# Kernel optimization log

Measured on AMD Instinct MI355X. Metric: run time of the kernel, lower is better.

The kernel has to match this reference:

```python
import jax, jax.numpy as jnp
import numpy as np

N = 200000          # nodes
E = 12_800_000      # edges (avg degree 64)
C = 4               # conv_out_channels == node_features
H = 32              # lstm_out_channels


def setup_inputs() -> dict:
    key = jax.random.key(0)
    ks = jax.random.split(key, 16)
    inv_c = 1.0 / np.sqrt(C)
    inv_h = 1.0 / np.sqrt(H)
    return {
        "x": jax.random.normal(ks[0], (N, C), jnp.float32),
        "edge_index": jax.random.randint(ks[1], (2, E), 0, N, dtype=jnp.int64),
        "edge_weight": jax.random.uniform(ks[2], (E,), jnp.float32),
        "h_0": 0.1 * jax.random.normal(ks[3], (1, N, H), jnp.float32),
        "c_0": 0.1 * jax.random.normal(ks[4], (1, N, H), jnp.float32),
        # GatedGraphConv (num_layers=1): weight[0] of shape [C, C]
        "conv_weight": inv_c * jax.random.normal(ks[5], (C, C), jnp.float32),
        # GRUCell(C, C) params (PyTorch layout: [3C, C], gate order r,z,n)
        "gru_w_ih": inv_c * jax.random.normal(ks[6], (3 * C, C), jnp.float32),
        "gru_w_hh": inv_c * jax.random.normal(ks[7], (3 * C, C), jnp.float32),
        "gru_b_ih": inv_c * jax.random.normal(ks[8], (3 * C,), jnp.float32),
        "gru_b_hh": inv_c * jax.random.normal(ks[9], (3 * C,), jnp.float32),
        # LSTM(C, H, 1 layer) params (PyTorch layout: [4H, *], gate order i,f,g,o)
        "lstm_w_ih": inv_h * jax.random.normal(ks[10], (4 * H, C), jnp.float32),
        "lstm_w_hh": inv_h * jax.random.normal(ks[11], (4 * H, H), jnp.float32),
        "lstm_b_ih": inv_h * jax.random.normal(ks[12], (4 * H,), jnp.float32),
        "lstm_b_hh": inv_h * jax.random.normal(ks[13], (4 * H,), jnp.float32),
        # Linear(32, 1)
        "lin_w": inv_h * jax.random.normal(ks[14], (1, H), jnp.float32),
        "lin_b": inv_h * jax.random.normal(ks[15], (1,), jnp.float32),
    }


def reference(x, edge_index, edge_weight, h_0, c_0,
              conv_weight, gru_w_ih, gru_w_hh, gru_b_ih, gru_b_hh,
              lstm_w_ih, lstm_w_hh, lstm_b_ih, lstm_b_hh, lin_w, lin_b):
    n = x.shape[0]
    src, dst = edge_index[0], edge_index[1]  # source j -> target i

    # ---- GatedGraphConv, 1 layer (in_dim == out_channels, no padding) ----
    m = x @ conv_weight                                   # [N, C]
    msg = m[src] * edge_weight[:, None]                   # [E, C] gather
    summed = jax.ops.segment_sum(msg, dst, num_segments=n)
    cnt = jax.ops.segment_sum(jnp.ones((msg.shape[0],), msg.dtype), dst,
                              num_segments=n)
    agg = summed / jnp.maximum(cnt, 1.0)[:, None]         # mean aggr (empty -> 0)

    # GRUCell(agg, x): r,z,n gate order
    gi = agg @ gru_w_ih.T + gru_b_ih
    gh = x @ gru_w_hh.T + gru_b_hh
    i_r, i_z, i_n = jnp.split(gi, 3, axis=1)
    h_r, h_z, h_n = jnp.split(gh, 3, axis=1)
    r = jax.nn.sigmoid(i_r + h_r)
    z = jax.nn.sigmoid(i_z + h_z)
    nn_ = jnp.tanh(i_n + r * h_n)
    h_conv = (1.0 - z) * nn_ + z * x                      # [N, C]

    # ---- LSTM: seq_len=1, batch=N, 1 layer; gate order i,f,g,o ----
    h_prev, c_prev = h_0[0], c_0[0]                       # [N, H]
    gates = h_conv @ lstm_w_ih.T + lstm_b_ih + h_prev @ lstm_w_hh.T + lstm_b_hh
    ig, fg, gg, og = jnp.split(gates, 4, axis=1)
    ig, fg, og = jax.nn.sigmoid(ig), jax.nn.sigmoid(fg), jax.nn.sigmoid(og)
    gg = jnp.tanh(gg)
    c_new = fg * c_prev + ig * gg
    h_new = og * jnp.tanh(c_new)                          # [N, H]

    # ---- relu + linear head ----
    out = jax.nn.relu(h_new) @ lin_w.T + lin_b            # [N, 1]
    return out, h_new[None], c_new[None]
```

## Files before the change

### kernel.cpp

```cpp
#include <hip/hip_runtime.h>
#include <math.h>

#define B_SHIFT 9
#define BMASK   511
#define CHUNK   16384
#define NTHR    256
#define AGG_THR 512

static __device__ __forceinline__ float sigf(float x) {
  return 1.0f / (1.0f + __expf(-x));
}
static __device__ __forceinline__ float tanhfast(float x) {
  return 2.0f / (1.0f + __expf(-2.0f * x)) - 1.0f;
}

__global__ void conv_m_kernel(const float* __restrict__ x,
                              const float* __restrict__ w,
                              float* __restrict__ m, int n) {
  int i = blockIdx.x * blockDim.x + threadIdx.x;
  if (i >= n) return;
  float4 xv = reinterpret_cast<const float4*>(x)[i];
  float4 mv;
  mv.x = xv.x * w[0] + xv.y * w[4] + xv.z * w[8]  + xv.w * w[12];
  mv.y = xv.x * w[1] + xv.y * w[5] + xv.z * w[9]  + xv.w * w[13];
  mv.z = xv.x * w[2] + xv.y * w[6] + xv.z * w[10] + xv.w * w[14];
  mv.w = xv.x * w[3] + xv.y * w[7] + xv.z * w[11] + xv.w * w[15];
  reinterpret_cast<float4*>(m)[i] = mv;
}


__global__ __launch_bounds__(NTHR) void hist_kernel(const int* __restrict__ dst,
                                                    int E, int B,
                                                    int* __restrict__ gCnt) {
  __shared__ int h[1024];
  for (int b = threadIdx.x; b < B; b += NTHR) h[b] = 0;
  __syncthreads();
  const int4* d4 = reinterpret_cast<const int4*>(dst);
  int i4base = (int)(((long long)blockIdx.x * CHUNK) >> 2);
  int lim4 = E >> 2;
#pragma unroll
  for (int j = 0; j < 16; ++j) {
    int i4 = i4base + j * NTHR + threadIdx.x;
    if (i4 < lim4) {
      int4 d = d4[i4];
      atomicAdd(&h[d.x >> B_SHIFT], 1);
      atomicAdd(&h[d.y >> B_SHIFT], 1);
      atomicAdd(&h[d.z >> B_SHIFT], 1);
      atomicAdd(&h[d.w >> B_SHIFT], 1);
    }
  }
  if (blockIdx.x == 0 && threadIdx.x == 0) {
    for (int e = E & ~3; e < E; ++e) atomicAdd(&h[dst[e] >> B_SHIFT], 1);
  }
  __syncthreads();
  for (int b = threadIdx.x; b < B; b += NTHR) {
    int c = h[b];
    if (c) atomicAdd(&gCnt[b], c);
  }
}

__global__ void scan_kernel(const int* __restrict__ gCnt, int B,
                            int* __restrict__ start, int* __restrict__ cursor) {
  __shared__ int s[1024];
  int t = threadIdx.x;
  int v = (t < B) ? gCnt[t] : 0;
  s[t] = v;
  __syncthreads();
  for (int off = 1; off < 1024; off <<= 1) {
    int u = (t >= off) ? s[t - off] : 0;
    __syncthreads();
    s[t] += u;
    __syncthreads();
  }
  if (t < B) {
    int excl = (t == 0) ? 0 : s[t - 1];
    start[t] = excl;
    cursor[t] = excl;
  }
  if (t == 0) start[B] = s[1023];
}

__global__ __launch_bounds__(NTHR) void bin_kernel(const int* __restrict__ ei,
                                                   const float* __restrict__ ew,
                                                   int E, int B,
                                                   int* __restrict__ cursor,
                                                   int2* __restrict__ binned) {
  __shared__ int h[1024];
  for (int b = threadIdx.x; b < B; b += NTHR) h[b] = 0;
  __syncthreads();
  const int* dst = ei + E;
  const int4* d4 = reinterpret_cast<const int4*>(dst);
  const int4* s4 = reinterpret_cast<const int4*>(ei);
  const float4* w4 = reinterpret_cast<const float4*>(ew);
  int i4base = (int)(((long long)blockIdx.x * CHUNK) >> 2);
  int lim4 = E >> 2;
#pragma unroll
  for (int j = 0; j < 16; ++j) {
    int i4 = i4base + j * NTHR + threadIdx.x;
    if (i4 < lim4) {
      int4 d = d4[i4];
      atomicAdd(&h[d.x >> B_SHIFT], 1);
      atomicAdd(&h[d.y >> B_SHIFT], 1);
      atomicAdd(&h[d.z >> B_SHIFT], 1);
      atomicAdd(&h[d.w >> B_SHIFT], 1);
    }
  }
  __syncthreads();
  for (int b = threadIdx.x; b < B; b += NTHR) {
    int c = h[b];
    if (c) h[b] = atomicAdd(&cursor[b], c);
  }
  __syncthreads();
#pragma unroll
  for (int j = 0; j < 16; ++j) {
    int i4 = i4base + j * NTHR + threadIdx.x;
    if (i4 < lim4) {
      int4 d = d4[i4];
      int4 s = s4[i4];
      float4 w = w4[i4];
      int p;
      p = atomicAdd(&h[d.x >> B_SHIFT], 1);
      binned[p] = make_int2((s.x << B_SHIFT) | (d.x & BMASK), __float_as_int(w.x));
      p = atomicAdd(&h[d.y >> B_SHIFT], 1);
      binned[p] = make_int2((s.y << B_SHIFT) | (d.y & BMASK), __float_as_int(w.y));
      p = atomicAdd(&h[d.z >> B_SHIFT], 1);
      binned[p] = make_int2((s.z << B_SHIFT) | (d.z & BMASK), __float_as_int(w.z));
      p = atomicAdd(&h[d.w >> B_SHIFT], 1);
      binned[p] = make_int2((s.w << B_SHIFT) | (d.w & BMASK), __float_as_int(w.w));
    }
  }
  if (blockIdx.x == 0 && threadIdx.x == 0) {
    for (int e = E & ~3; e < E; ++e) {
      int d = dst[e];
      int p = atomicAdd(&cursor[d >> B_SHIFT], 1);
      binned[p] = make_int2((ei[e] << B_SHIFT) | (d & BMASK), __float_as_int(ew[e]));
    }
  }
}

__global__ __launch_bounds__(AGG_THR) void agg_node_kernel(
    const float* __restrict__ x, const float* __restrict__ m,
    const int2* __restrict__ binned, const int* __restrict__ start,
    const float* __restrict__ h0, const float* __restrict__ c0,
    const float* __restrict__ gwi, const float* __restrict__ gwh,
    const float* __restrict__ gbi, const float* __restrict__ gbh,
    const float* __restrict__ lwi, const float* __restrict__ lwh,
    const float* __restrict__ lbi, const float* __restrict__ lbh,
    const float* __restrict__ linw, const float* __restrict__ linb,
    float* __restrict__ out, float* __restrict__ hout, float* __restrict__ cout,
    int n) {
  __shared__ float acc[512 * 5];
  int tid = threadIdx.x;
  for (int idx = tid; idx < 512 * 5; idx += AGG_THR) acc[idx] = 0.0f;
  __syncthreads();

  int s = start[blockIdx.x], e = start[blockIdx.x + 1];
  const float4* m4 = reinterpret_cast<const float4*>(m);
  int i = s + tid;
  for (; i + AGG_THR < e; i += 2 * AGG_THR) {
    int2 r0 = binned[i];
    int2 r1 = binned[i + AGG_THR];
    float4 mv0 = m4[r0.x >> B_SHIFT];
    float4 mv1 = m4[r1.x >> B_SHIFT];
    float w0 = __int_as_float(r0.y);
    float w1 = __int_as_float(r1.y);
    int dl0 = (r0.x & BMASK) * 5;
    int dl1 = (r1.x & BMASK) * 5;
    atomicAdd(&acc[dl0 + 0], mv0.x * w0);
    atomicAdd(&acc[dl0 + 1], mv0.y * w0);
    atomicAdd(&acc[dl0 + 2], mv0.z * w0);
    atomicAdd(&acc[dl0 + 3], mv0.w * w0);
    atomicAdd(&acc[dl0 + 4], 1.0f);
    atomicAdd(&acc[dl1 + 0], mv1.x * w1);
    atomicAdd(&acc[dl1 + 1], mv1.y * w1);
    atomicAdd(&acc[dl1 + 2], mv1.z * w1);
    atomicAdd(&acc[dl1 + 3], mv1.w * w1);
    atomicAdd(&acc[dl1 + 4], 1.0f);
  }
  if (i < e) {
    int2 r = binned[i];
    int src = r.x >> B_SHIFT;
    int dl = (r.x & BMASK) * 5;
    float w = __int_as_float(r.y);
    float4 mv = m4[src];
    atomicAdd(&acc[dl + 0], mv.x * w);
    atomicAdd(&acc[dl + 1], mv.y * w);
    atomicAdd(&acc[dl + 2], mv.z * w);
    atomicAdd(&acc[dl + 3], mv.w * w);
    atomicAdd(&acc[dl + 4], 1.0f);
  }
  __syncthreads();

  int node = (blockIdx.x << B_SHIFT) + tid;
  if (node >= n) return;

  float inv = 1.0f / fmaxf(acc[tid * 5 + 4], 1.0f);
  float agg[4] = {acc[tid * 5 + 0] * inv, acc[tid * 5 + 1] * inv,
                  acc[tid * 5 + 2] * inv, acc[tid * 5 + 3] * inv};
  float4 xv = reinterpret_cast<const float4*>(x)[node];
  float xa[4] = {xv.x, xv.y, xv.z, xv.w};

  float hc[4];
#pragma unroll
  for (int c = 0; c < 4; ++c) {
    float gi_r = gbi[c],     gh_r = gbh[c];
    float gi_z = gbi[4 + c], gh_z = gbh[4 + c];
    float gi_n = gbi[8 + c], gh_n = gbh[8 + c];
#pragma unroll
    for (int k = 0; k < 4; ++k) {
      gi_r += agg[k] * gwi[c * 4 + k];       gh_r += xa[k] * gwh[c * 4 + k];
      gi_z += agg[k] * gwi[(4 + c) * 4 + k]; gh_z += xa[k] * gwh[(4 + c) * 4 + k];
      gi_n += agg[k] * gwi[(8 + c) * 4 + k]; gh_n += xa[k] * gwh[(8 + c) * 4 + k];
    }
    float r = sigf(gi_r + gh_r);
    float z = sigf(gi_z + gh_z);
    float nn = tanhfast(gi_n + r * gh_n);
    hc[c] = (1.0f - z) * nn + z * xa[c];
  }

  const float4* h04 = reinterpret_cast<const float4*>(h0) + (size_t)node * 8;
  const float4* c04 = reinterpret_cast<const float4*>(c0) + (size_t)node * 8;
  float hp[32];
#pragma unroll
  for (int q = 0; q < 8; ++q) {
    float4 hv = h04[q];
    hp[q * 4 + 0] = hv.x; hp[q * 4 + 1] = hv.y;
    hp[q * 4 + 2] = hv.z; hp[q * 4 + 3] = hv.w;
  }
  const float4* wih4 = reinterpret_cast<const float4*>(lwi);
  const float4* whh4 = reinterpret_cast<const float4*>(lwh);
  float oacc = linb[0];
  float4* hout4 = reinterpret_cast<float4*>(hout) + (size_t)node * 8;
  float4* cout4 = reinterpret_cast<float4*>(cout) + (size_t)node * 8;

#pragma unroll
  for (int jc = 0; jc < 8; ++jc) {
    float4 cpv = c04[jc];
    float cpa[4] = {cpv.x, cpv.y, cpv.z, cpv.w};
    float hn[4], cn[4];
#pragma unroll
    for (int jj = 0; jj < 4; ++jj) {
      int j = jc * 4 + jj;
      float gI = lbi[j]      + lbh[j];
      float gF = lbi[32 + j] + lbh[32 + j];
      float gG = lbi[64 + j] + lbh[64 + j];
      float gO = lbi[96 + j] + lbh[96 + j];
      float4 wi = wih4[j], wf = wih4[32 + j], wg = wih4[64 + j], wo = wih4[96 + j];
      gI += hc[0] * wi.x + hc[1] * wi.y + hc[2] * wi.z + hc[3] * wi.w;
      gF += hc[0] * wf.x + hc[1] * wf.y + hc[2] * wf.z + hc[3] * wf.w;
      gG += hc[0] * wg.x + hc[1] * wg.y + hc[2] * wg.z + hc[3] * wg.w;
      gO += hc[0] * wo.x + hc[1] * wo.y + hc[2] * wo.z + hc[3] * wo.w;
#pragma unroll
      for (int q = 0; q < 8; ++q) {
        float4 a = whh4[j * 8 + q];
        float4 b = whh4[(32 + j) * 8 + q];
        float4 g = whh4[(64 + j) * 8 + q];
        float4 o = whh4[(96 + j) * 8 + q];
        float p0 = hp[q * 4 + 0], p1 = hp[q * 4 + 1];
        float p2 = hp[q * 4 + 2], p3 = hp[q * 4 + 3];
        gI += p0 * a.x + p1 * a.y + p2 * a.z + p3 * a.w;
        gF += p0 * b.x + p1 * b.y + p2 * b.z + p3 * b.w;
        gG += p0 * g.x + p1 * g.y + p2 * g.z + p3 * g.w;
        gO += p0 * o.x + p1 * o.y + p2 * o.z + p3 * o.w;
      }
      float ig = sigf(gI), fg = sigf(gF), og = sigf(gO), gg = tanhfast(gG);
      float cnew = fg * cpa[jj] + ig * gg;
      float hnew = og * tanhfast(cnew);
      cn[jj] = cnew; hn[jj] = hnew;
      oacc += fmaxf(hnew, 0.0f) * linw[j];
    }
    hout4[jc] = make_float4(hn[0], hn[1], hn[2], hn[3]);
    cout4[jc] = make_float4(cn[0], cn[1], cn[2], cn[3]);
  }
  out[node] = oacc;
}


__global__ void edge_kernel(const int* __restrict__ ei,
                            const float* __restrict__ ew,
                            const float* __restrict__ m,
                            float* __restrict__ summed,
                            float* __restrict__ cnt, int E) {
  int t = blockIdx.x * blockDim.x + threadIdx.x;
  int e0 = t * 4;
  const float4* m4 = reinterpret_cast<const float4*>(m);
  for (int e = e0; e < E && e < e0 + 4; ++e) {
    int s = ei[e], d = ei[E + e];
    float w = ew[e];
    float4 mv = m4[s];
    float* p = summed + 4ll * d;
    unsafeAtomicAdd(p + 0, mv.x * w);
    unsafeAtomicAdd(p + 1, mv.y * w);
    unsafeAtomicAdd(p + 2, mv.z * w);
    unsafeAtomicAdd(p + 3, mv.w * w);
    unsafeAtomicAdd(cnt + d, 1.0f);
  }
}

__global__ __launch_bounds__(NTHR) void node_kernel(
    const float* __restrict__ x, const float* __restrict__ summed,
    const float* __restrict__ cnt,
    const float* __restrict__ h0, const float* __restrict__ c0,
    const float* __restrict__ gwi, const float* __restrict__ gwh,
    const float* __restrict__ gbi, const float* __restrict__ gbh,
    const float* __restrict__ lwi, const float* __restrict__ lwh,
    const float* __restrict__ lbi, const float* __restrict__ lbh,
    const float* __restrict__ linw, const float* __restrict__ linb,
    float* __restrict__ out, float* __restrict__ hout, float* __restrict__ cout,
    int n) {
  int i = blockIdx.x * blockDim.x + threadIdx.x;
  if (i >= n) return;
  float4 sv = reinterpret_cast<const float4*>(summed)[i];
  float inv = 1.0f / fmaxf(cnt[i], 1.0f);
  float agg[4] = {sv.x * inv, sv.y * inv, sv.z * inv, sv.w * inv};
  float4 xv = reinterpret_cast<const float4*>(x)[i];
  float xa[4] = {xv.x, xv.y, xv.z, xv.w};
  float hc[4];
#pragma unroll
  for (int c = 0; c < 4; ++c) {
    float gi_r = gbi[c],     gh_r = gbh[c];
    float gi_z = gbi[4 + c], gh_z = gbh[4 + c];
    float gi_n = gbi[8 + c], gh_n = gbh[8 + c];
#pragma unroll
    for (int k = 0; k < 4; ++k) {
      gi_r += agg[k] * gwi[c * 4 + k];       gh_r += xa[k] * gwh[c * 4 + k];
      gi_z += agg[k] * gwi[(4 + c) * 4 + k]; gh_z += xa[k] * gwh[(4 + c) * 4 + k];
      gi_n += agg[k] * gwi[(8 + c) * 4 + k]; gh_n += xa[k] * gwh[(8 + c) * 4 + k];
    }
    float r = sigf(gi_r + gh_r);
    float z = sigf(gi_z + gh_z);
    float nn = tanhfast(gi_n + r * gh_n);
    hc[c] = (1.0f - z) * nn + z * xa[c];
  }
  const float4* h04 = reinterpret_cast<const float4*>(h0) + (size_t)i * 8;
  const float4* c04 = reinterpret_cast<const float4*>(c0) + (size_t)i * 8;
  float hp[32];
#pragma unroll
  for (int q = 0; q < 8; ++q) {
    float4 hv = h04[q];
    hp[q * 4 + 0] = hv.x; hp[q * 4 + 1] = hv.y;
    hp[q * 4 + 2] = hv.z; hp[q * 4 + 3] = hv.w;
  }
  const float4* wih4 = reinterpret_cast<const float4*>(lwi);
  const float4* whh4 = reinterpret_cast<const float4*>(lwh);
  float oacc = linb[0];
  float4* hout4 = reinterpret_cast<float4*>(hout) + (size_t)i * 8;
  float4* cout4 = reinterpret_cast<float4*>(cout) + (size_t)i * 8;
#pragma unroll
  for (int jc = 0; jc < 8; ++jc) {
    float4 cpv = c04[jc];
    float cpa[4] = {cpv.x, cpv.y, cpv.z, cpv.w};
    float hn[4], cn[4];
#pragma unroll
    for (int jj = 0; jj < 4; ++jj) {
      int j = jc * 4 + jj;
      float gI = lbi[j]      + lbh[j];
      float gF = lbi[32 + j] + lbh[32 + j];
      float gG = lbi[64 + j] + lbh[64 + j];
      float gO = lbi[96 + j] + lbh[96 + j];
      float4 wi = wih4[j], wf = wih4[32 + j], wg = wih4[64 + j], wo = wih4[96 + j];
      gI += hc[0] * wi.x + hc[1] * wi.y + hc[2] * wi.z + hc[3] * wi.w;
      gF += hc[0] * wf.x + hc[1] * wf.y + hc[2] * wf.z + hc[3] * wf.w;
      gG += hc[0] * wg.x + hc[1] * wg.y + hc[2] * wg.z + hc[3] * wg.w;
      gO += hc[0] * wo.x + hc[1] * wo.y + hc[2] * wo.z + hc[3] * wo.w;
#pragma unroll
      for (int q = 0; q < 8; ++q) {
        float4 a = whh4[j * 8 + q];
        float4 b = whh4[(32 + j) * 8 + q];
        float4 g = whh4[(64 + j) * 8 + q];
        float4 o = whh4[(96 + j) * 8 + q];
        float p0 = hp[q * 4 + 0], p1 = hp[q * 4 + 1];
        float p2 = hp[q * 4 + 2], p3 = hp[q * 4 + 3];
        gI += p0 * a.x + p1 * a.y + p2 * a.z + p3 * a.w;
        gF += p0 * b.x + p1 * b.y + p2 * b.z + p3 * b.w;
        gG += p0 * g.x + p1 * g.y + p2 * g.z + p3 * g.w;
        gO += p0 * o.x + p1 * o.y + p2 * o.z + p3 * o.w;
      }
      float ig = sigf(gI), fg = sigf(gF), og = sigf(gO), gg = tanhfast(gG);
      float cnew = fg * cpa[jj] + ig * gg;
      float hnew = og * tanhfast(cnew);
      cn[jj] = cnew; hn[jj] = hnew;
      oacc += fmaxf(hnew, 0.0f) * linw[j];
    }
    hout4[jc] = make_float4(hn[0], hn[1], hn[2], hn[3]);
    cout4[jc] = make_float4(cn[0], cn[1], cn[2], cn[3]);
  }
  out[i] = oacc;
}

extern "C" void kernel_launch(void* const* d_in, const int* in_sizes, int n_in,
                              void* d_out, int out_size, void* d_ws, size_t ws_size,
                              hipStream_t stream) {
  const float* x     = (const float*)d_in[0];
  const int*   ei    = (const int*)d_in[1];
  const float* ew    = (const float*)d_in[2];
  const float* h0    = (const float*)d_in[3];
  const float* c0    = (const float*)d_in[4];
  const float* convw = (const float*)d_in[5];
  const float* gwi   = (const float*)d_in[6];
  const float* gwh   = (const float*)d_in[7];
  const float* gbi   = (const float*)d_in[8];
  const float* gbh   = (const float*)d_in[9];
  const float* lwi   = (const float*)d_in[10];
  const float* lwh   = (const float*)d_in[11];
  const float* lbi   = (const float*)d_in[12];
  const float* lbh   = (const float*)d_in[13];
  const float* linw  = (const float*)d_in[14];
  const float* linb  = (const float*)d_in[15];

  int n = in_sizes[0] / 4;
  int E = in_sizes[1] / 2;

  float* out  = (float*)d_out;
  float* hout = out + n;
  float* cout = hout + (size_t)n * 32;

  int B = (n + BMASK) >> B_SHIFT;
  size_t need = (size_t)E * 8 + (size_t)n * 16 + ((size_t)3 * B + 2) * 4 + 64;

  if (B <= 1024 && ws_size >= need) {
    int2*  binned = (int2*)d_ws;
    float* m      = (float*)(binned + E);
    int*   gCnt   = (int*)(m + (size_t)n * 4);
    int*   start  = gCnt + B;
    int*   cursor = start + B + 1;

    hipMemsetAsync(gCnt, 0, (size_t)B * sizeof(int), stream);
    conv_m_kernel<<<(n + NTHR - 1) / NTHR, NTHR, 0, stream>>>(x, convw, m, n);

    int nbBlocks = (E + CHUNK - 1) / CHUNK;
    hist_kernel<<<nbBlocks, NTHR, 0, stream>>>(ei + E, E, B, gCnt);
    scan_kernel<<<1, 1024, 0, stream>>>(gCnt, B, start, cursor);
    bin_kernel<<<nbBlocks, NTHR, 0, stream>>>(ei, ew, E, B, cursor, binned);

    agg_node_kernel<<<B, AGG_THR, 0, stream>>>(
        x, m, binned, start, h0, c0,
        gwi, gwh, gbi, gbh, lwi, lwh, lbi, lbh, linw, linb,
        out, hout, cout, n);
  } else {
    float* m      = (float*)d_ws;
    float* summed = m + (size_t)n * 4;
    float* cntp   = summed + (size_t)n * 4;
    hipMemsetAsync(summed, 0, (size_t)n * 5 * sizeof(float), stream);
    conv_m_kernel<<<(n + NTHR - 1) / NTHR, NTHR, 0, stream>>>(x, convw, m, n);
    int et = (E + 3) / 4;
    edge_kernel<<<(et + NTHR - 1) / NTHR, NTHR, 0, stream>>>(ei, ew, m, summed, cntp, E);
    node_kernel<<<(n + NTHR - 1) / NTHR, NTHR, 0, stream>>>(
        x, summed, cntp, h0, c0,
        gwi, gwh, gbi, gbh, lwi, lwh, lbi, lbh, linw, linb,
        out, hout, cout, n);
  }
}
```

Before: 1.058 ms.

## Split fused edge-aggregation/LSTM kernel and halve bin size for more blocks

Splits the fused aggregation-plus-node-update kernel into an LDS-atomic edge aggregation kernel writing mean aggregates to workspace and a separate per-node GRU/LSTM kernel. Bin size drops from 512 to 256 nodes, doubling the number of aggregation blocks, with a 4-way unrolled edge loop and workgroup-scoped relaxed LDS atomics. This targets low block count and occupancy limits from the register-heavy LSTM tail sharing a kernel with the atomics loop. It costs an extra global write/read of the aggregate array, one more launch, and more bins in the histogram/scan.

```diff
diff --git a/kernel.cpp b/kernel.cpp
--- a/kernel.cpp
+++ b/kernel.cpp
@@ -1,11 +1,13 @@
 #include <hip/hip_runtime.h>
 #include <math.h>
 
-#define B_SHIFT 9
-#define BMASK   511
+#define B_SHIFT 8
+#define BMASK   255
 #define CHUNK   16384
 #define NTHR    256
-#define AGG_THR 512
+
+#define LDSADD(p, v) __hip_atomic_fetch_add((p), (v), __ATOMIC_RELAXED, \
+                                            __HIP_MEMORY_SCOPE_WORKGROUP)
 
 static __device__ __forceinline__ float sigf(float x) {
   return 1.0f / (1.0f + __expf(-x));
@@ -138,9 +140,65 @@
   }
 }
 
-__global__ __launch_bounds__(AGG_THR) void agg_node_kernel(
-    const float* __restrict__ x, const float* __restrict__ m,
-    const int2* __restrict__ binned, const int* __restrict__ start,
+__global__ __launch_bounds__(NTHR) void edge_agg_kernel(
+    const float* __restrict__ m, const int2* __restrict__ binned,
+    const int* __restrict__ start, float* __restrict__ aggOut, int n) {
+  __shared__ float acc[NTHR * 5];
+  int tid = threadIdx.x;
+#pragma unroll
+  for (int k = 0; k < 5; ++k) acc[k * NTHR + tid] = 0.0f;
+  __syncthreads();
+
+  int s = start[blockIdx.x], e = start[blockIdx.x + 1];
+  const float4* m4 = reinterpret_cast<const float4*>(m);
+  int i = s + tid;
+  for (; i + 3 * NTHR < e; i += 4 * NTHR) {
+    int2 r0 = binned[i];
+    int2 r1 = binned[i + NTHR];
+    int2 r2 = binned[i + 2 * NTHR];
+    int2 r3 = binned[i + 3 * NTHR];
+    float4 v0 = m4[r0.x >> B_SHIFT];
+    float4 v1 = m4[r1.x >> B_SHIFT];
+    float4 v2 = m4[r2.x >> B_SHIFT];
+    float4 v3 = m4[r3.x >> B_SHIFT];
+    float w0 = __int_as_float(r0.y), w1 = __int_as_float(r1.y);
+    float w2 = __int_as_float(r2.y), w3 = __int_as_float(r3.y);
+    int a0 = (r0.x & BMASK) * 5, a1 = (r1.x & BMASK) * 5;
+    int a2 = (r2.x & BMASK) * 5, a3 = (r3.x & BMASK) * 5;
+    LDSADD(&acc[a0 + 0], v0.x * w0); LDSADD(&acc[a0 + 1], v0.y * w0);
+    LDSADD(&acc[a0 + 2], v0.z * w0); LDSADD(&acc[a0 + 3], v0.w * w0);
+    LDSADD(&acc[a0 + 4], 1.0f);
+    LDSADD(&acc[a1 + 0], v1.x * w1); LDSADD(&acc[a1 + 1], v1.y * w1);
+    LDSADD(&acc[a1 + 2], v1.z * w1); LDSADD(&acc[a1 + 3], v1.w * w1);
+    LDSADD(&acc[a1 + 4], 1.0f);
+    LDSADD(&acc[a2 + 0], v2.x * w2); LDSADD(&acc[a2 + 1], v2.y * w2);
+    LDSADD(&acc[a2 + 2], v2.z * w2); LDSADD(&acc[a2 + 3], v2.w * w2);
+    LDSADD(&acc[a2 + 4], 1.0f);
+    LDSADD(&acc[a3 + 0], v3.x * w3); LDSADD(&acc[a3 + 1], v3.y * w3);
+    LDSADD(&acc[a3 + 2], v3.z * w3); LDSADD(&acc[a3 + 3], v3.w * w3);
+    LDSADD(&acc[a3 + 4], 1.0f);
+  }
+  for (; i < e; i += NTHR) {
+    int2 r = binned[i];
+    float4 v = m4[r.x >> B_SHIFT];
+    float w = __int_as_float(r.y);
+    int a = (r.x & BMASK) * 5;
+    LDSADD(&acc[a + 0], v.x * w); LDSADD(&acc[a + 1], v.y * w);
+    LDSADD(&acc[a + 2], v.z * w); LDSADD(&acc[a + 3], v.w * w);
+    LDSADD(&acc[a + 4], 1.0f);
+  }
+  __syncthreads();
+
+  int node = (blockIdx.x << B_SHIFT) + tid;
+  if (node >= n) return;
+  float inv = 1.0f / fmaxf(acc[tid * 5 + 4], 1.0f);
+  reinterpret_cast<float4*>(aggOut)[node] =
+      make_float4(acc[tid * 5 + 0] * inv, acc[tid * 5 + 1] * inv,
+                  acc[tid * 5 + 2] * inv, acc[tid * 5 + 3] * inv);
+}
+
+__global__ __launch_bounds__(NTHR) void node_kernel2(
+    const float* __restrict__ x, const float* __restrict__ aggIn,
     const float* __restrict__ h0, const float* __restrict__ c0,
     const float* __restrict__ gwi, const float* __restrict__ gwh,
     const float* __restrict__ gbi, const float* __restrict__ gbh,
@@ -149,55 +207,11 @@
     const float* __restrict__ linw, const float* __restrict__ linb,
     float* __restrict__ out, float* __restrict__ hout, float* __restrict__ cout,
     int n) {
-  __shared__ float acc[512 * 5];
-  int tid = threadIdx.x;
-  for (int idx = tid; idx < 512 * 5; idx += AGG_THR) acc[idx] = 0.0f;
-  __syncthreads();
-
-  int s = start[blockIdx.x], e = start[blockIdx.x + 1];
-  const float4* m4 = reinterpret_cast<const float4*>(m);
-  int i = s + tid;
-  for (; i + AGG_THR < e; i += 2 * AGG_THR) {
-    int2 r0 = binned[i];
-    int2 r1 = binned[i + AGG_THR];
-    float4 mv0 = m4[r0.x >> B_SHIFT];
-    float4 mv1 = m4[r1.x >> B_SHIFT];
-    float w0 = __int_as_float(r0.y);
-    float w1 = __int_as_float(r1.y);
-    int dl0 = (r0.x & BMASK) * 5;
-    int dl1 = (r1.x & BMASK) * 5;
-    atomicAdd(&acc[dl0 + 0], mv0.x * w0);
-    atomicAdd(&acc[dl0 + 1], mv0.y * w0);
-    atomicAdd(&acc[dl0 + 2], mv0.z * w0);
-    atomicAdd(&acc[dl0 + 3], mv0.w * w0);
-    atomicAdd(&acc[dl0 + 4], 1.0f);
-    atomicAdd(&acc[dl1 + 0], mv1.x * w1);
-    atomicAdd(&acc[dl1 + 1], mv1.y * w1);
-    atomicAdd(&acc[dl1 + 2], mv1.z * w1);
-    atomicAdd(&acc[dl1 + 3], mv1.w * w1);
-    atomicAdd(&acc[dl1 + 4], 1.0f);
-  }
-  if (i < e) {
-    int2 r = binned[i];
-    int src = r.x >> B_SHIFT;
-    int dl = (r.x & BMASK) * 5;
-    float w = __int_as_float(r.y);
-    float4 mv = m4[src];
-    atomicAdd(&acc[dl + 0], mv.x * w);
-    atomicAdd(&acc[dl + 1], mv.y * w);
-    atomicAdd(&acc[dl + 2], mv.z * w);
-    atomicAdd(&acc[dl + 3], mv.w * w);
-    atomicAdd(&acc[dl + 4], 1.0f);
-  }
-  __syncthreads();
-
-  int node = (blockIdx.x << B_SHIFT) + tid;
-  if (node >= n) return;
-
-  float inv = 1.0f / fmaxf(acc[tid * 5 + 4], 1.0f);
-  float agg[4] = {acc[tid * 5 + 0] * inv, acc[tid * 5 + 1] * inv,
-                  acc[tid * 5 + 2] * inv, acc[tid * 5 + 3] * inv};
-  float4 xv = reinterpret_cast<const float4*>(x)[node];
+  int i = blockIdx.x * blockDim.x + threadIdx.x;
+  if (i >= n) return;
+  float4 av = reinterpret_cast<const float4*>(aggIn)[i];
+  float agg[4] = {av.x, av.y, av.z, av.w};
+  float4 xv = reinterpret_cast<const float4*>(x)[i];
   float xa[4] = {xv.x, xv.y, xv.z, xv.w};
 
   float hc[4];
@@ -218,8 +232,8 @@
     hc[c] = (1.0f - z) * nn + z * xa[c];
   }
 
-  const float4* h04 = reinterpret_cast<const float4*>(h0) + (size_t)node * 8;
-  const float4* c04 = reinterpret_cast<const float4*>(c0) + (size_t)node * 8;
+  const float4* h04 = reinterpret_cast<const float4*>(h0) + (size_t)i * 8;
+  const float4* c04 = reinterpret_cast<const float4*>(c0) + (size_t)i * 8;
   float hp[32];
 #pragma unroll
   for (int q = 0; q < 8; ++q) {
@@ -230,8 +244,8 @@
   const float4* wih4 = reinterpret_cast<const float4*>(lwi);
   const float4* whh4 = reinterpret_cast<const float4*>(lwh);
   float oacc = linb[0];
-  float4* hout4 = reinterpret_cast<float4*>(hout) + (size_t)node * 8;
-  float4* cout4 = reinterpret_cast<float4*>(cout) + (size_t)node * 8;
+  float4* hout4 = reinterpret_cast<float4*>(hout) + (size_t)i * 8;
+  float4* cout4 = reinterpret_cast<float4*>(cout) + (size_t)i * 8;
 
 #pragma unroll
   for (int jc = 0; jc < 8; ++jc) {
@@ -272,7 +286,7 @@
     hout4[jc] = make_float4(hn[0], hn[1], hn[2], hn[3]);
     cout4[jc] = make_float4(cn[0], cn[1], cn[2], cn[3]);
   }
-  out[node] = oacc;
+  out[i] = oacc;
 }
 
 
@@ -416,12 +430,13 @@
   float* cout = hout + (size_t)n * 32;
 
   int B = (n + BMASK) >> B_SHIFT;
-  size_t need = (size_t)E * 8 + (size_t)n * 16 + ((size_t)3 * B + 2) * 4 + 64;
+  size_t need = (size_t)E * 8 + (size_t)n * 32 + ((size_t)3 * B + 2) * 4 + 64;
 
   if (B <= 1024 && ws_size >= need) {
     int2*  binned = (int2*)d_ws;
     float* m      = (float*)(binned + E);
-    int*   gCnt   = (int*)(m + (size_t)n * 4);
+    float* aggOut = m + (size_t)n * 4;
+    int*   gCnt   = (int*)(aggOut + (size_t)n * 4);
     int*   start  = gCnt + B;
     int*   cursor = start + B + 1;
 
@@ -433,8 +448,9 @@
     scan_kernel<<<1, 1024, 0, stream>>>(gCnt, B, start, cursor);
     bin_kernel<<<nbBlocks, NTHR, 0, stream>>>(ei, ew, E, B, cursor, binned);
 
-    agg_node_kernel<<<B, AGG_THR, 0, stream>>>(
-        x, m, binned, start, h0, c0,
+    edge_agg_kernel<<<B, NTHR, 0, stream>>>(m, binned, start, aggOut, n);
+    node_kernel2<<<(n + NTHR - 1) / NTHR, NTHR, 0, stream>>>(
+        x, aggOut, h0, c0,
         gwi, gwh, gbi, gbh, lwi, lwh, lbi, lbh, linw, linb,
         out, hout, cout, n);
   } else {
```

Result: slower. 1.157 ms (+9.3%).
